# Optimization experiments

Measured on AMD Instinct MI355X. Metric: run time of the kernel, lower is better.

Reference implementation:

```python
import jax, jax.numpy as jnp
import numpy as np

N_NODES = 102400
N_EDGES = 1638400
DIMS = [128, 64, 32, 1]  # decoder_dim=128, decoder_l=3, last layer -> 1


def setup_inputs() -> dict:
    key = jax.random.key(0)
    ks = jax.random.split(key, 10)
    inp = {
        'b_z': jax.random.normal(ks[0], (N_NODES, DIMS[0]), jnp.float32),
        'src': jax.random.randint(ks[1], (N_EDGES,), 0, N_NODES, jnp.int64 if jax.config.jax_enable_x64 else jnp.int32),
        'dst': jax.random.randint(ks[2], (N_EDGES,), 0, N_NODES, jnp.int64 if jax.config.jax_enable_x64 else jnp.int32),
        'edge_weight': jax.random.uniform(ks[3], (N_EDGES,), jnp.float32),
        'b_size': 100,
    }
    # GraphConv weights: W [in, out], bias [out] (DGL xavier init; randn ok for ref)
    for i in range(3):
        inp[f'W{i}'] = jax.random.normal(ks[4 + i], (DIMS[i], DIMS[i + 1]), jnp.float32) * (1.0 / np.sqrt(DIMS[i]))
        inp[f'b{i}'] = jnp.zeros((DIMS[i + 1],), jnp.float32)
    return inp


def _gcn_layer(h, src, dst, ew, W, b, activate):
    n = h.shape[0]
    ones = jnp.ones((src.shape[0],), h.dtype)
    # norm='both': symmetric degree normalization with plain (unweighted) degrees
    out_deg = jnp.clip(jax.ops.segment_sum(ones, src, num_segments=n), 1.0)
    in_deg = jnp.clip(jax.ops.segment_sum(ones, dst, num_segments=n), 1.0)
    h = h * (out_deg ** -0.5)[:, None]
    h = h @ W  # in_feats > out_feats: transform before aggregation (DGL order)
    msg = h[src] * ew[:, None]           # [E, out] edge-weighted gather
    agg = jax.ops.segment_sum(msg, dst, num_segments=n)  # scatter-add
    agg = agg * (in_deg ** -0.5)[:, None] + b
    return jnp.tanh(agg) if activate else agg


def reference(b_z, src, dst, edge_weight, b_size, W0, b0, W1, b1, W2, b2):
    h = b_z
    h = _gcn_layer(h, src, dst, edge_weight, W0, b0, True)
    h = _gcn_layer(h, src, dst, edge_weight, W1, b1, True)
    h = _gcn_layer(h, src, dst, edge_weight, W2, b2, False)
    return h.reshape(b_size, -1)
```

## Files before the change

### kernel.cpp

```cpp
#include <hip/hip_runtime.h>
#include <hip/hip_fp16.h>
#include <math.h>

#define N_NODES 102400
#define N_EDGES 1638400
#define NB 100
#define PB 256
#define EPB (N_EDGES/PB)

__global__ __launch_bounds__(256) void histA_kernel(const int* __restrict__ src, const int* __restrict__ dst,
                                                    int* __restrict__ histD, int* __restrict__ histS) {
    __shared__ int hD[NB], hS[NB];
    int tid = threadIdx.x;
    if (tid < NB) { hD[tid] = 0; hS[tid] = 0; }
    __syncthreads();
    int base = blockIdx.x * EPB;
    for (int i = tid; i < EPB; i += 256) {
        atomicAdd(&hD[dst[base + i] >> 10], 1);
        atomicAdd(&hS[src[base + i] >> 10], 1);
    }
    __syncthreads();
    if (tid < NB) {
        histD[blockIdx.x * NB + tid] = hD[tid];
        histS[blockIdx.x * NB + tid] = hS[tid];
    }
}

__global__ __launch_bounds__(256) void scanB_kernel(const int* __restrict__ histD, const int* __restrict__ histS,
                                                    int* __restrict__ offD, int* __restrict__ offS,
                                                    int* __restrict__ coarseD, int* __restrict__ coarseS) {
    __shared__ int totD[NB], totS[NB], baseD[NB + 1], baseS[NB + 1];
    int t = threadIdx.x;
    if (t < NB) { int s = 0; for (int k = 0; k < PB; k++) s += histD[k * NB + t]; totD[t] = s; }
    else if (t >= 128 && t < 128 + NB) { int j = t - 128; int s = 0; for (int k = 0; k < PB; k++) s += histS[k * NB + j]; totS[j] = s; }
    __syncthreads();
    if (t == 0)   { int r = 0; for (int j = 0; j < NB; j++) { baseD[j] = r; r += totD[j]; } baseD[NB] = r; }
    if (t == 128) { int r = 0; for (int j = 0; j < NB; j++) { baseS[j] = r; r += totS[j]; } baseS[NB] = r; }
    __syncthreads();
    if (t < NB) { int r = baseD[t]; for (int k = 0; k < PB; k++) { offD[k * NB + t] = r; r += histD[k * NB + t]; } }
    else if (t >= 128 && t < 128 + NB) { int j = t - 128; int r = baseS[j]; for (int k = 0; k < PB; k++) { offS[k * NB + j] = r; r += histS[k * NB + j]; } }
    if (t <= NB) coarseD[t] = baseD[t];
    if (t >= 128 && t <= 128 + NB) coarseS[t - 128] = baseS[t - 128];
}

__global__ __launch_bounds__(256) void partC_kernel(const int* __restrict__ src, const int* __restrict__ dst,
                                                    const float* __restrict__ ew,
                                                    const int* __restrict__ offD, const int* __restrict__ offS,
                                                    int2* __restrict__ partD, int* __restrict__ partS) {
    __shared__ int cD[NB], cS[NB];
    int tid = threadIdx.x;
    if (tid < NB) { cD[tid] = offD[blockIdx.x * NB + tid]; cS[tid] = offS[blockIdx.x * NB + tid]; }
    __syncthreads();
    int base = blockIdx.x * EPB;
    for (int i = tid; i < EPB; i += 256) {
        int s = src[base + i], d = dst[base + i];
        float w = ew[base + i];
        int p = atomicAdd(&cD[d >> 10], 1);
        partD[p] = make_int2(s | ((d & 1023) << 17), __float_as_int(w));
        int q = atomicAdd(&cS[s >> 10], 1);
        partS[q] = s & 1023;
    }
}

__global__ __launch_bounds__(1024) void fineS_kernel(const int* __restrict__ partS, const int* __restrict__ coarseS,
                                                     float* __restrict__ outdeg_inv) {
    __shared__ int hist[1024];
    int tid = threadIdx.x;
    hist[tid] = 0;
    __syncthreads();
    int beg = coarseS[blockIdx.x], end = coarseS[blockIdx.x + 1];
    for (int i = beg + tid; i < end; i += 1024) atomicAdd(&hist[partS[i]], 1);
    __syncthreads();
    outdeg_inv[blockIdx.x * 1024 + tid] = 1.0f / sqrtf((float)max(hist[tid], 1));
}

__global__ __launch_bounds__(1024) void fineD_kernel(const int2* __restrict__ partD, const int* __restrict__ coarseD,
                                                     const float* __restrict__ outdeg_inv,
                                                     int2* __restrict__ edge_perm, int* __restrict__ row_off,
                                                     float* __restrict__ indeg_inv) {
    __shared__ int hist[1024], cursor[1024];
    __shared__ int wsum[16];
    int tid = threadIdx.x, lane = tid & 63, wid = tid >> 6;
    hist[tid] = 0;
    __syncthreads();
    int beg = coarseD[blockIdx.x], end = coarseD[blockIdx.x + 1];
    for (int i = beg + tid; i < end; i += 1024) atomicAdd(&hist[(partD[i].x >> 17) & 1023], 1);
    __syncthreads();
    int v = hist[tid];
    int x = v;
    #pragma unroll
    for (int s = 1; s < 64; s <<= 1) { int t = __shfl_up(x, s, 64); if (lane >= s) x += t; }
    if (lane == 63) wsum[wid] = x;
    __syncthreads();
    if (wid == 0) {
        int ws = (lane < 16) ? wsum[lane] : 0;
        int y = ws;
        #pragma unroll
        for (int s = 1; s < 16; s <<= 1) { int t = __shfl_up(y, s, 64); if (lane >= s) y += t; }
        if (lane < 16) wsum[lane] = y - ws;
    }
    __syncthreads();
    int ex = wsum[wid] + x - v;
    cursor[tid] = beg + ex;
    int node = blockIdx.x * 1024 + tid;
    row_off[node] = beg + ex;
    indeg_inv[node] = 1.0f / sqrtf((float)max(v, 1));
    if (blockIdx.x == NB - 1 && tid == 0) row_off[N_NODES] = N_EDGES;
    __syncthreads();
    for (int i = beg + tid; i < end; i += 1024) {
        int2 t2 = partD[i];
        int d = (t2.x >> 17) & 1023, s = t2.x & 0x1FFFF;
        int p = atomicAdd(&cursor[d], 1);
        float w = __int_as_float(t2.y) * outdeg_inv[s];
        edge_perm[p] = make_int2(s, __float_as_int(w));
    }
}

template<int K, int C, int RN>
__global__ __launch_bounds__(256) void gemm_tile_kernel(
    const float* __restrict__ h, const float* __restrict__ W, __half* __restrict__ out) {
    constexpr int BM = 64;
    constexpr int RM = 4;
    constexpr int KC = 64;
    constexpr int TX = C / RN;
    constexpr int TY = BM / RM;
    static_assert(TX * TY == 256, "bad tile");
    static_assert(RN == 4, "fp16 epilogue assumes RN==4");

    __shared__ float Ws[K * C];
    __shared__ float Hs[KC][BM + 4];

    const int tid = threadIdx.x;
    const long brow = (long)blockIdx.x * BM;

    for (int i = tid; i < K * C; i += 256) Ws[i] = W[i];

    const int tx = tid % TX;
    const int ty = tid / TX;
    float acc[RM][RN] = {};

    const int lr = tid % 16;
    const int lk = tid / 16;

    for (int kc = 0; kc < K; kc += KC) {
        __syncthreads();
        #pragma unroll
        for (int p0 = 0; p0 < BM; p0 += 16) {
            const int r = p0 + lr;
            const float4 hv = *(const float4*)(h + (brow + r) * K + kc + lk * 4);
            Hs[lk * 4 + 0][r] = hv.x;
            Hs[lk * 4 + 1][r] = hv.y;
            Hs[lk * 4 + 2][r] = hv.z;
            Hs[lk * 4 + 3][r] = hv.w;
        }
        __syncthreads();

        #pragma unroll
        for (int k = 0; k < KC; ++k) {
            const float4 a4 = *(const float4*)&Hs[k][ty * RM];
            const float av[RM] = {a4.x, a4.y, a4.z, a4.w};
            float b[RN];
            *(float4*)b = *(const float4*)&Ws[(kc + k) * C + tx * RN];
            #pragma unroll
            for (int i = 0; i < RM; ++i)
                #pragma unroll
                for (int j = 0; j < RN; ++j)
                    acc[i][j] += av[i] * b[j];
        }
    }

    #pragma unroll
    for (int i = 0; i < RM; ++i) {
        const long row = brow + ty * RM + i;
        __half2 p01 = __floats2half2_rn(acc[i][0], acc[i][1]);
        __half2 p23 = __floats2half2_rn(acc[i][2], acc[i][3]);
        int2 packed = make_int2(*(int*)&p01, *(int*)&p23);
        *(int2*)(out + row * C + tx * RN) = packed;
    }
}

__global__ __launch_bounds__(256) void agg64_gemm_kernel(
    const __half* __restrict__ ht, const int* __restrict__ row_off,
    const int2* __restrict__ ep, const float* __restrict__ indeg_inv,
    const float* __restrict__ b0, const float* __restrict__ W1,
    __half* __restrict__ ht1, int N) {
    __shared__ float W1s[64 * 32];
    __shared__ float h1s[4][64];
    int tid = threadIdx.x;
    {
        const float4* W1v = (const float4*)W1;
        float4* W1sv = (float4*)W1s;
        W1sv[tid] = W1v[tid];
        W1sv[tid + 256] = W1v[tid + 256];
    }
    __syncthreads();

    int wave = (blockIdx.x * blockDim.x + tid) >> 6;
    int lane = tid & 63;
    if (wave >= N) return;
    int chunk = lane & 15;
    int eslot = lane >> 4;
    int beg = row_off[wave], end = row_off[wave + 1];

    float4 a0 = {0, 0, 0, 0}, a1 = {0, 0, 0, 0};
    for (int e = beg; e < end; e += 8) {
        int ei0 = e + eslot, ei1 = e + 4 + eslot;
        int2 d0 = ep[min(ei0, end - 1)];
        int2 d1 = ep[min(ei1, end - 1)];
        float w0 = (ei0 < end) ? __int_as_float(d0.y) : 0.0f;
        float w1 = (ei1 < end) ? __int_as_float(d1.y) : 0.0f;
        int2 r0 = *(const int2*)(ht + (long)d0.x * 64 + chunk * 4);
        int2 r1 = *(const int2*)(ht + (long)d1.x * 64 + chunk * 4);
        float2 f0a = __half22float2(*(__half2*)&r0.x);
        float2 f0b = __half22float2(*(__half2*)&r0.y);
        float2 f1a = __half22float2(*(__half2*)&r1.x);
        float2 f1b = __half22float2(*(__half2*)&r1.y);
        a0.x += f0a.x * w0; a0.y += f0a.y * w0; a0.z += f0b.x * w0; a0.w += f0b.y * w0;
        a1.x += f1a.x * w1; a1.y += f1a.y * w1; a1.z += f1b.x * w1; a1.w += f1b.y * w1;
    }
    a0.x += a1.x; a0.y += a1.y; a0.z += a1.z; a0.w += a1.w;
    #pragma unroll
    for (int s = 16; s <= 32; s <<= 1) {
        a0.x += __shfl_xor(a0.x, s, 64);
        a0.y += __shfl_xor(a0.y, s, 64);
        a0.z += __shfl_xor(a0.z, s, 64);
        a0.w += __shfl_xor(a0.w, s, 64);
    }
    int wv = tid >> 6;
    if (eslot == 0) {
        float sc = indeg_inv[wave];
        float4 b = *(const float4*)(b0 + chunk * 4);
        float4 v;
        v.x = tanhf(a0.x * sc + b.x);
        v.y = tanhf(a0.y * sc + b.y);
        v.z = tanhf(a0.z * sc + b.z);
        v.w = tanhf(a0.w * sc + b.w);
        *(float4*)&h1s[wv][chunk * 4] = v;
    }
    int c = lane & 31, half = lane >> 5;
    float t = 0.0f;
    #pragma unroll
    for (int j4 = 0; j4 < 8; ++j4) {
        int k = half * 32 + j4 * 4;
        float4 hh = *(const float4*)&h1s[wv][k];
        t += hh.x * W1s[(k + 0) * 32 + c];
        t += hh.y * W1s[(k + 1) * 32 + c];
        t += hh.z * W1s[(k + 2) * 32 + c];
        t += hh.w * W1s[(k + 3) * 32 + c];
    }
    t += __shfl_xor(t, 32, 64);
    if (half == 0) ht1[(long)wave * 32 + c] = __float2half_rn(t);
}

__global__ void agg32_dot_kernel(const __half* __restrict__ ht, const int* __restrict__ row_off,
                                 const int2* __restrict__ ep,
                                 const float* __restrict__ indeg_inv, const float* __restrict__ bias,
                                 const float* __restrict__ W2, float* __restrict__ ht2, int N) {
    int wave = (blockIdx.x * blockDim.x + threadIdx.x) >> 6;
    int lane = threadIdx.x & 63;
    if (wave >= N) return;
    int chunk = lane & 7;
    int eslot = lane >> 3;
    int beg = row_off[wave], end = row_off[wave + 1];
    float4 a0 = {0, 0, 0, 0}, a1 = {0, 0, 0, 0};
    for (int e = beg; e < end; e += 16) {
        int ei0 = e + eslot, ei1 = e + 8 + eslot;
        int2 d0 = ep[min(ei0, end - 1)];
        int2 d1 = ep[min(ei1, end - 1)];
        float w0 = (ei0 < end) ? __int_as_float(d0.y) : 0.0f;
        float w1 = (ei1 < end) ? __int_as_float(d1.y) : 0.0f;
        int2 r0 = *(const int2*)(ht + (long)d0.x * 32 + chunk * 4);
        int2 r1 = *(const int2*)(ht + (long)d1.x * 32 + chunk * 4);
        float2 f0a = __half22float2(*(__half2*)&r0.x);
        float2 f0b = __half22float2(*(__half2*)&r0.y);
        float2 f1a = __half22float2(*(__half2*)&r1.x);
        float2 f1b = __half22float2(*(__half2*)&r1.y);
        a0.x += f0a.x * w0; a0.y += f0a.y * w0; a0.z += f0b.x * w0; a0.w += f0b.y * w0;
        a1.x += f1a.x * w1; a1.y += f1a.y * w1; a1.z += f1b.x * w1; a1.w += f1b.y * w1;
    }
    a0.x += a1.x; a0.y += a1.y; a0.z += a1.z; a0.w += a1.w;
    #pragma unroll
    for (int s = 8; s <= 32; s <<= 1) {
        a0.x += __shfl_xor(a0.x, s, 64);
        a0.y += __shfl_xor(a0.y, s, 64);
        a0.z += __shfl_xor(a0.z, s, 64);
        a0.w += __shfl_xor(a0.w, s, 64);
    }
    float sc = indeg_inv[wave];
    float4 b = *(const float4*)(bias + chunk * 4);
    float4 w2 = *(const float4*)(W2 + chunk * 4);
    float t = tanhf(a0.x * sc + b.x) * w2.x
            + tanhf(a0.y * sc + b.y) * w2.y
            + tanhf(a0.z * sc + b.z) * w2.z
            + tanhf(a0.w * sc + b.w) * w2.w;
    t += __shfl_xor(t, 1, 64);
    t += __shfl_xor(t, 2, 64);
    t += __shfl_xor(t, 4, 64);
    if (lane == 0) ht2[wave] = t;
}

__global__ void agg1_kernel(const float* __restrict__ ht2, const int* __restrict__ row_off,
                            const int2* __restrict__ ep,
                            const float* __restrict__ indeg_inv, const float* __restrict__ bias,
                            float* __restrict__ out, int N) {
    int wave = (blockIdx.x * blockDim.x + threadIdx.x) >> 6;
    int lane = threadIdx.x & 63;
    int sub = lane >> 4;
    int slot = lane & 15;
    int node = wave * 4 + sub;
    if (node >= N) return;
    int beg = row_off[node], end = row_off[node + 1];
    float acc = 0.0f;
    for (int e = beg + slot; e < end; e += 16) {
        int2 t = ep[e];
        acc += ht2[t.x] * __int_as_float(t.y);
    }
    #pragma unroll
    for (int s = 1; s <= 8; s <<= 1) acc += __shfl_xor(acc, s, 64);
    if (slot == 0) out[node] = acc * indeg_inv[node] + bias[0];
}

extern "C" void kernel_launch(void* const* d_in, const int* in_sizes, int n_in,
                              void* d_out, int out_size, void* d_ws, size_t ws_size,
                              hipStream_t stream) {
    const float* b_z = (const float*)d_in[0];
    const int*   src = (const int*)d_in[1];
    const int*   dst = (const int*)d_in[2];
    const float* ew  = (const float*)d_in[3];
    const float* W0 = (const float*)d_in[5];
    const float* b0 = (const float*)d_in[6];
    const float* W1 = (const float*)d_in[7];
    const float* b1 = (const float*)d_in[8];
    const float* W2 = (const float*)d_in[9];
    const float* b2 = (const float*)d_in[10];
    float* out = (float*)d_out;

    const int N = N_NODES;
    const int E = N_EDGES;

    char* p = (char*)d_ws;
    int*   row_off    = (int*)p;            p += (size_t)(N + 4) * 4;
    float* outdeg_inv = (float*)p;          p += (size_t)N * 4;
    float* indeg_inv  = (float*)p;          p += (size_t)N * 4;
    int*   histD      = (int*)p;            p += (size_t)PB * NB * 4;
    int*   histS      = (int*)p;            p += (size_t)PB * NB * 4;
    int*   offD       = (int*)p;            p += (size_t)PB * NB * 4;
    int*   offS       = (int*)p;            p += (size_t)PB * NB * 4;
    int*   coarseD    = (int*)p;            p += (size_t)(NB + 4) * 4;
    int*   coarseS    = (int*)p;            p += (size_t)(NB + 4) * 4;
    int2*  edge_perm  = (int2*)p;           p += (size_t)E * 8;
    float* bufA       = (float*)p;          p += (size_t)N * 64 * 4;
    float* bufB       = (float*)p;
    int2*   partD = (int2*)bufA;
    int*    partS = (int*)bufB;
    __half* ht    = (__half*)bufA;
    __half* ht1   = (__half*)bufB;
    float*  ht2   = bufA;

    histA_kernel<<<PB, 256, 0, stream>>>(src, dst, histD, histS);
    scanB_kernel<<<1, 256, 0, stream>>>(histD, histS, offD, offS, coarseD, coarseS);
    partC_kernel<<<PB, 256, 0, stream>>>(src, dst, ew, offD, offS, partD, partS);
    fineS_kernel<<<NB, 1024, 0, stream>>>(partS, coarseS, outdeg_inv);
    fineD_kernel<<<NB, 1024, 0, stream>>>(partD, coarseD, outdeg_inv, edge_perm, row_off, indeg_inv);

    gemm_tile_kernel<128, 64, 4><<<N / 64, 256, 0, stream>>>(b_z, W0, ht);

    agg64_gemm_kernel<<<N / 4, 256, 0, stream>>>(ht, row_off, edge_perm, indeg_inv, b0, W1, ht1, N);

    agg32_dot_kernel<<<N / 4, 256, 0, stream>>>(ht1, row_off, edge_perm, indeg_inv, b1, W2, ht2, N);

    agg1_kernel<<<N / 16, 256, 0, stream>>>(ht2, row_off, edge_perm, indeg_inv, b2, out, N);
}
```

Before: 340.8 us.

## Sort edges by source slice within each node and unroll gather loops

The fine CSR build now keeps per-node histograms split into 8 source-index slices, so each node's edges are ordered by coarse source range. This is meant to give the aggregation gathers better cache locality. The 64-wide and 32-wide aggregation kernels also get a full-tile fast path without bounds masking, with the 64-wide one issuing four gathers per iteration for more memory-level parallelism. In exchange the build uses 8x the shared memory and does an extra prefix pass, which lowers occupancy in that kernel.

```diff
diff --git a/kernel.cpp b/kernel.cpp
--- a/kernel.cpp
+++ b/kernel.cpp
@@ -7,6 +7,7 @@
 #define NB 100
 #define PB 256
 #define EPB (N_EDGES/PB)
+#define NSL 8
 
 __global__ __launch_bounds__(256) void histA_kernel(const int* __restrict__ src, const int* __restrict__ dst,
                                                     int* __restrict__ histD, int* __restrict__ histS) {
@@ -78,15 +79,24 @@
                                                      const float* __restrict__ outdeg_inv,
                                                      int2* __restrict__ edge_perm, int* __restrict__ row_off,
                                                      float* __restrict__ indeg_inv) {
-    __shared__ int hist[1024], cursor[1024];
+    __shared__ int hist[NSL * 1024];
     __shared__ int wsum[16];
     int tid = threadIdx.x, lane = tid & 63, wid = tid >> 6;
-    hist[tid] = 0;
+    #pragma unroll
+    for (int j = 0; j < NSL; ++j) hist[j * 1024 + tid] = 0;
     __syncthreads();
     int beg = coarseD[blockIdx.x], end = coarseD[blockIdx.x + 1];
-    for (int i = beg + tid; i < end; i += 1024) atomicAdd(&hist[(partD[i].x >> 17) & 1023], 1);
-    __syncthreads();
-    int v = hist[tid];
+    for (int i = beg + tid; i < end; i += 1024) {
+        int xk = partD[i].x;
+        int node = (xk >> 17) & 1023;
+        int sl = (xk & 0x1FFFF) >> 14;
+        atomicAdd(&hist[sl * 1024 + node], 1);
+    }
+    __syncthreads();
+    int pre[NSL];
+    int v = 0;
+    #pragma unroll
+    for (int j = 0; j < NSL; ++j) { pre[j] = v; v += hist[j * 1024 + tid]; }
     int x = v;
     #pragma unroll
     for (int s = 1; s < 64; s <<= 1) { int t = __shfl_up(x, s, 64); if (lane >= s) x += t; }
@@ -100,17 +110,20 @@
         if (lane < 16) wsum[lane] = y - ws;
     }
     __syncthreads();
-    int ex = wsum[wid] + x - v;
-    cursor[tid] = beg + ex;
+    int node_start = beg + wsum[wid] + x - v;
     int node = blockIdx.x * 1024 + tid;
-    row_off[node] = beg + ex;
+    row_off[node] = node_start;
     indeg_inv[node] = 1.0f / sqrtf((float)max(v, 1));
     if (blockIdx.x == NB - 1 && tid == 0) row_off[N_NODES] = N_EDGES;
     __syncthreads();
+    #pragma unroll
+    for (int j = 0; j < NSL; ++j) hist[j * 1024 + tid] = node_start + pre[j];
+    __syncthreads();
     for (int i = beg + tid; i < end; i += 1024) {
         int2 t2 = partD[i];
-        int d = (t2.x >> 17) & 1023, s = t2.x & 0x1FFFF;
-        int p = atomicAdd(&cursor[d], 1);
+        int nd = (t2.x >> 17) & 1023, s = t2.x & 0x1FFFF;
+        int sl = s >> 14;
+        int p = atomicAdd(&hist[sl * 1024 + nd], 1);
         float w = __int_as_float(t2.y) * outdeg_inv[s];
         edge_perm[p] = make_int2(s, __float_as_int(w));
     }
@@ -203,20 +216,34 @@
     int beg = row_off[wave], end = row_off[wave + 1];
 
     float4 a0 = {0, 0, 0, 0}, a1 = {0, 0, 0, 0};
-    for (int e = beg; e < end; e += 8) {
-        int ei0 = e + eslot, ei1 = e + 4 + eslot;
-        int2 d0 = ep[min(ei0, end - 1)];
-        int2 d1 = ep[min(ei1, end - 1)];
-        float w0 = (ei0 < end) ? __int_as_float(d0.y) : 0.0f;
-        float w1 = (ei1 < end) ? __int_as_float(d1.y) : 0.0f;
+    int e = beg;
+    for (; e + 16 <= end; e += 16) {
+        int2 d0 = ep[e + eslot];
+        int2 d1 = ep[e + 4 + eslot];
+        int2 d2 = ep[e + 8 + eslot];
+        int2 d3 = ep[e + 12 + eslot];
         int2 r0 = *(const int2*)(ht + (long)d0.x * 64 + chunk * 4);
         int2 r1 = *(const int2*)(ht + (long)d1.x * 64 + chunk * 4);
-        float2 f0a = __half22float2(*(__half2*)&r0.x);
-        float2 f0b = __half22float2(*(__half2*)&r0.y);
-        float2 f1a = __half22float2(*(__half2*)&r1.x);
-        float2 f1b = __half22float2(*(__half2*)&r1.y);
+        int2 r2 = *(const int2*)(ht + (long)d2.x * 64 + chunk * 4);
+        int2 r3 = *(const int2*)(ht + (long)d3.x * 64 + chunk * 4);
+        float w0 = __int_as_float(d0.y), w1 = __int_as_float(d1.y);
+        float w2 = __int_as_float(d2.y), w3 = __int_as_float(d3.y);
+        float2 f0a = __half22float2(*(__half2*)&r0.x), f0b = __half22float2(*(__half2*)&r0.y);
+        float2 f1a = __half22float2(*(__half2*)&r1.x), f1b = __half22float2(*(__half2*)&r1.y);
+        float2 f2a = __half22float2(*(__half2*)&r2.x), f2b = __half22float2(*(__half2*)&r2.y);
+        float2 f3a = __half22float2(*(__half2*)&r3.x), f3b = __half22float2(*(__half2*)&r3.y);
         a0.x += f0a.x * w0; a0.y += f0a.y * w0; a0.z += f0b.x * w0; a0.w += f0b.y * w0;
         a1.x += f1a.x * w1; a1.y += f1a.y * w1; a1.z += f1b.x * w1; a1.w += f1b.y * w1;
+        a0.x += f2a.x * w2; a0.y += f2a.y * w2; a0.z += f2b.x * w2; a0.w += f2b.y * w2;
+        a1.x += f3a.x * w3; a1.y += f3a.y * w3; a1.z += f3b.x * w3; a1.w += f3b.y * w3;
+    }
+    for (; e < end; e += 4) {
+        int ei = e + eslot;
+        int2 d0 = ep[min(ei, end - 1)];
+        float w0 = (ei < end) ? __int_as_float(d0.y) : 0.0f;
+        int2 r0 = *(const int2*)(ht + (long)d0.x * 64 + chunk * 4);
+        float2 f0a = __half22float2(*(__half2*)&r0.x), f0b = __half22float2(*(__half2*)&r0.y);
+        a0.x += f0a.x * w0; a0.y += f0a.y * w0; a0.z += f0b.x * w0; a0.w += f0b.y * w0;
     }
     a0.x += a1.x; a0.y += a1.y; a0.z += a1.z; a0.w += a1.w;
     #pragma unroll
@@ -263,20 +290,25 @@
     int eslot = lane >> 3;
     int beg = row_off[wave], end = row_off[wave + 1];
     float4 a0 = {0, 0, 0, 0}, a1 = {0, 0, 0, 0};
-    for (int e = beg; e < end; e += 16) {
-        int ei0 = e + eslot, ei1 = e + 8 + eslot;
-        int2 d0 = ep[min(ei0, end - 1)];
-        int2 d1 = ep[min(ei1, end - 1)];
-        float w0 = (ei0 < end) ? __int_as_float(d0.y) : 0.0f;
-        float w1 = (ei1 < end) ? __int_as_float(d1.y) : 0.0f;
+    int e = beg;
+    for (; e + 16 <= end; e += 16) {
+        int2 d0 = ep[e + eslot];
+        int2 d1 = ep[e + 8 + eslot];
         int2 r0 = *(const int2*)(ht + (long)d0.x * 32 + chunk * 4);
         int2 r1 = *(const int2*)(ht + (long)d1.x * 32 + chunk * 4);
-        float2 f0a = __half22float2(*(__half2*)&r0.x);
-        float2 f0b = __half22float2(*(__half2*)&r0.y);
-        float2 f1a = __half22float2(*(__half2*)&r1.x);
-        float2 f1b = __half22float2(*(__half2*)&r1.y);
+        float w0 = __int_as_float(d0.y), w1 = __int_as_float(d1.y);
+        float2 f0a = __half22float2(*(__half2*)&r0.x), f0b = __half22float2(*(__half2*)&r0.y);
+        float2 f1a = __half22float2(*(__half2*)&r1.x), f1b = __half22float2(*(__half2*)&r1.y);
         a0.x += f0a.x * w0; a0.y += f0a.y * w0; a0.z += f0b.x * w0; a0.w += f0b.y * w0;
         a1.x += f1a.x * w1; a1.y += f1a.y * w1; a1.z += f1b.x * w1; a1.w += f1b.y * w1;
+    }
+    for (; e < end; e += 8) {
+        int ei = e + eslot;
+        int2 d0 = ep[min(ei, end - 1)];
+        float w0 = (ei < end) ? __int_as_float(d0.y) : 0.0f;
+        int2 r0 = *(const int2*)(ht + (long)d0.x * 32 + chunk * 4);
+        float2 f0a = __half22float2(*(__half2*)&r0.x), f0b = __half22float2(*(__half2*)&r0.y);
+        a0.x += f0a.x * w0; a0.y += f0a.y * w0; a0.z += f0b.x * w0; a0.w += f0b.y * w0;
     }
     a0.x += a1.x; a0.y += a1.y; a0.z += a1.z; a0.w += a1.w;
     #pragma unroll
```

New measurement: 344.5 us. About the same (+1.1%).
